# Optimization experiments

Measured on AMD Instinct MI355X. Metric: run time of the kernel, lower is better.

Reference implementation:

```python
import jax, jax.numpy as jnp
import numpy as np

B, A, RF, F = 4096, 128, 128, 128  # batch, max_atom, res_n_features, n_features


def setup_inputs() -> dict:
    key = jax.random.key(0)
    k1, k2, k3, k4 = jax.random.split(key, 4)
    node_features = jax.random.normal(k1, (B, A, F), dtype=jnp.float32)
    residual_features = jax.random.normal(k2, (B, A, RF), dtype=jnp.float32)
    # Glorot-style init for the residual transform weight
    scale = jnp.sqrt(6.0 / (RF + F)).astype(jnp.float32)
    w = jax.random.uniform(k3, (RF, F), dtype=jnp.float32, minval=-scale, maxval=scale)
    # mol_slice[g] = [n_atoms_g, n_features]; atom counts vary per graph (ragged)
    atoms = jax.random.randint(k4, (B,), 1, A + 1, dtype=jnp.int64)
    mol_slice = jnp.stack([atoms, jnp.full((B,), F, dtype=jnp.int64)], axis=1)
    return {"node_features": node_features, "residual_features": residual_features,
            "w": w, "mol_slice": mol_slice}


def reference(node_features, residual_features, w, mol_slice):
    # Original: per-graph slice to [M_g, F], x_res @ w + x, pad back to max_atom,
    # then relu. Equivalent masked batched form: rows >= M_g become zeros.
    M = mol_slice[:, 0]  # [B] atom counts
    row_mask = (jnp.arange(A)[None, :] < M[:, None])[:, :, None]  # [B, A, 1]
    y = jnp.einsum('bar,rf->baf', residual_features, w) + node_features  # [B, A, F]
    return jnp.where(row_mask, jax.nn.relu(y), jnp.zeros((), dtype=y.dtype))
```

## Files before the change

kernel.cpp:

```cpp
#include <hip/hip_runtime.h>


typedef __bf16 bf16x8 __attribute__((ext_vector_type(8)));
typedef float f32x4 __attribute__((ext_vector_type(4)));

static_assert(sizeof(bf16x8) == 16, "bf16x8 must be 16B");
static_assert(sizeof(f32x4) == 16, "f32x4 must be 16B");

__global__ __launch_bounds__(256) void wT_kernel(const float* __restrict__ w,
                                                 __bf16* __restrict__ wT) {
    int i = blockIdx.x * 256 + threadIdx.x;
    int f = i >> 7;
    int r = i & 127;
    wT[i] = (__bf16)w[r * 128 + f];
}

__global__ __launch_bounds__(256) void blockend_kernel(
    const float* __restrict__ node,
    const float* __restrict__ resid,
    const __bf16* __restrict__ wT,
    const int*   __restrict__ mol,
    float*       __restrict__ out)
{
    const int b    = blockIdx.x;
    const int t    = threadIdx.x;
    const int wave = t >> 6;
    const int lane = t & 63;
    const int quad = lane >> 4;
    const int m16  = lane & 15;

    const int M      = mol[2 * b];
    const int a_base = wave * 32;

    const size_t base = (size_t)b * (128 * 128);
    float* outW = out + base + (size_t)a_base * 128;

    if (M <= a_base) {
        f32x4 z = {0.f, 0.f, 0.f, 0.f};
        f32x4* p = (f32x4*)outW;
#pragma unroll
        for (int it = 0; it < 16; ++it)
            p[it * 64 + lane] = z;
        return;
    }

    const float* residW = resid + base + (size_t)a_base * 128;
    const float* nodeW  = node  + base + (size_t)a_base * 128;

    f32x4 acc[2][8];
#pragma unroll
    for (int nt = 0; nt < 2; ++nt)
#pragma unroll
        for (int ft = 0; ft < 8; ++ft)
            acc[nt][ft] = (f32x4){0.f, 0.f, 0.f, 0.f};

#pragma unroll
    for (int kk = 0; kk < 4; ++kk) {
        const int k0 = kk * 32 + quad * 8;

        bf16x8 rfrag[2];
#pragma unroll
        for (int nt = 0; nt < 2; ++nt) {
            const float* ap = residW + (nt * 16 + m16) * 128 + k0;
            f32x4 lo = *(const f32x4*)ap;
            f32x4 hi = *(const f32x4*)(ap + 4);
            bf16x8 v;
            v[0] = (__bf16)lo[0]; v[1] = (__bf16)lo[1];
            v[2] = (__bf16)lo[2]; v[3] = (__bf16)lo[3];
            v[4] = (__bf16)hi[0]; v[5] = (__bf16)hi[1];
            v[6] = (__bf16)hi[2]; v[7] = (__bf16)hi[3];
            rfrag[nt] = v;
        }

#pragma unroll
        for (int ft = 0; ft < 8; ++ft) {
            bf16x8 wfrag = *(const bf16x8*)(wT + (ft * 16 + m16) * 128 + k0);
#pragma unroll
            for (int nt = 0; nt < 2; ++nt)
                acc[nt][ft] = __builtin_amdgcn_mfma_f32_16x16x32_bf16(
                    wfrag, rfrag[nt], acc[nt][ft], 0, 0, 0);
        }
    }

#pragma unroll
    for (int nt = 0; nt < 2; ++nt) {
        const int a_local = nt * 16 + m16;
        const bool active = (a_base + a_local) < M;
#pragma unroll
        for (int ft = 0; ft < 8; ++ft) {
            const int off = a_local * 128 + ft * 16 + quad * 4;
            f32x4 v = {0.f, 0.f, 0.f, 0.f};
            if (active) {
                f32x4 nd = *(const f32x4*)(nodeW + off);
#pragma unroll
                for (int i = 0; i < 4; ++i) {
                    float x = acc[nt][ft][i] + nd[i];
                    v[i] = x > 0.f ? x : 0.f;
                }
            }
            *(f32x4*)(outW + off) = v;
        }
    }
}

extern "C" void kernel_launch(void* const* d_in, const int* in_sizes, int n_in,
                              void* d_out, int out_size, void* d_ws, size_t ws_size,
                              hipStream_t stream) {
    const float* node  = (const float*)d_in[0];
    const float* resid = (const float*)d_in[1];
    const float* w     = (const float*)d_in[2];
    const int*   mol   = (const int*)d_in[3];
    float*       out   = (float*)d_out;
    __bf16*      wT    = (__bf16*)d_ws;

    wT_kernel<<<64, 256, 0, stream>>>(w, wT);
    blockend_kernel<<<4096, 256, 0, stream>>>(node, resid, wT, mol, out);
}
```

Measured before the change: 575.1 us.

## Stage weights in LDS, process two graphs per block, skip masked row loads

```diff
diff --git a/kernel.cpp b/kernel.cpp
--- a/kernel.cpp
+++ b/kernel.cpp
@@ -7,6 +7,8 @@
 static_assert(sizeof(bf16x8) == 16, "bf16x8 must be 16B");
 static_assert(sizeof(f32x4) == 16, "f32x4 must be 16B");
 
+#define PB 2
+
 __global__ __launch_bounds__(256) void wT_kernel(const float* __restrict__ w,
                                                  __bf16* __restrict__ wT) {
     int i = blockIdx.x * 256 + threadIdx.x;
@@ -15,90 +17,113 @@
     wT[i] = (__bf16)w[r * 128 + f];
 }
 
-__global__ __launch_bounds__(256) void blockend_kernel(
+__global__ __launch_bounds__(256, 4) void blockend_kernel(
     const float* __restrict__ node,
     const float* __restrict__ resid,
-    const __bf16* __restrict__ wT,
+    const __bf16* __restrict__ wTg,
     const int*   __restrict__ mol,
     float*       __restrict__ out)
 {
-    const int b    = blockIdx.x;
+    __shared__ bf16x8 wlds[2048];
+
     const int t    = threadIdx.x;
     const int wave = t >> 6;
     const int lane = t & 63;
     const int quad = lane >> 4;
     const int m16  = lane & 15;
 
-    const int M      = mol[2 * b];
+#pragma unroll
+    for (int i = 0; i < 8; ++i) {
+        int c   = t + i * 256;
+        int f   = c >> 4;
+        int pos = c & 15;
+        bf16x8 v = *(const bf16x8*)(wTg + c * 8);
+        int s = (f >> 4) * 256 + (pos >> 2) * 64 + (pos & 3) * 16 + (f & 15);
+        wlds[s] = v;
+    }
+    __syncthreads();
+
     const int a_base = wave * 32;
 
-    const size_t base = (size_t)b * (128 * 128);
-    float* outW = out + base + (size_t)a_base * 128;
+    for (int mi = 0; mi < PB; ++mi) {
+        const int b = blockIdx.x * PB + mi;
+        const int M = mol[2 * b];
+        const size_t base = (size_t)b * (128 * 128);
+        float* outW = out + base + (size_t)a_base * 128;
 
-    if (M <= a_base) {
-        f32x4 z = {0.f, 0.f, 0.f, 0.f};
-        f32x4* p = (f32x4*)outW;
+        if (M <= a_base) {
+            f32x4 z = {0.f, 0.f, 0.f, 0.f};
+            f32x4* p = (f32x4*)outW;
 #pragma unroll
-        for (int it = 0; it < 16; ++it)
-            p[it * 64 + lane] = z;
-        return;
-    }
+            for (int it = 0; it < 16; ++it)
+                __builtin_nontemporal_store(z, p + it * 64 + lane);
+            continue;
+        }
 
-    const float* residW = resid + base + (size_t)a_base * 128;
-    const float* nodeW  = node  + base + (size_t)a_base * 128;
+        bf16x8 rfrag[2][4];
+#pragma unroll
+        for (int nt = 0; nt < 2; ++nt) {
+            const int row  = a_base + nt * 16 + m16;
+            const bool act = row < M;
+            const float* rp = resid + base + (size_t)row * 128 + quad * 8;
+#pragma unroll
+            for (int kk = 0; kk < 4; ++kk) {
+                f32x4 lo = {0.f, 0.f, 0.f, 0.f};
+                f32x4 hi = {0.f, 0.f, 0.f, 0.f};
+                if (act) {
+                    lo = *(const f32x4*)(rp + kk * 32);
+                    hi = *(const f32x4*)(rp + kk * 32 + 4);
+                }
+                bf16x8 v;
+                v[0] = (__bf16)lo[0]; v[1] = (__bf16)lo[1];
+                v[2] = (__bf16)lo[2]; v[3] = (__bf16)lo[3];
+                v[4] = (__bf16)hi[0]; v[5] = (__bf16)hi[1];
+                v[6] = (__bf16)hi[2]; v[7] = (__bf16)hi[3];
+                rfrag[nt][kk] = v;
+            }
+        }
 
-    f32x4 acc[2][8];
-#pragma unroll
-    for (int nt = 0; nt < 2; ++nt)
-#pragma unroll
-        for (int ft = 0; ft < 8; ++ft)
-            acc[nt][ft] = (f32x4){0.f, 0.f, 0.f, 0.f};
+        const float* nodeW = node + base + (size_t)a_base * 128;
 
 #pragma unroll
-    for (int kk = 0; kk < 4; ++kk) {
-        const int k0 = kk * 32 + quad * 8;
-
-        bf16x8 rfrag[2];
+        for (int h = 0; h < 2; ++h) {
+            f32x4 acc[2][4];
 #pragma unroll
-        for (int nt = 0; nt < 2; ++nt) {
-            const float* ap = residW + (nt * 16 + m16) * 128 + k0;
-            f32x4 lo = *(const f32x4*)ap;
-            f32x4 hi = *(const f32x4*)(ap + 4);
-            bf16x8 v;
-            v[0] = (__bf16)lo[0]; v[1] = (__bf16)lo[1];
-            v[2] = (__bf16)lo[2]; v[3] = (__bf16)lo[3];
-            v[4] = (__bf16)hi[0]; v[5] = (__bf16)hi[1];
-            v[6] = (__bf16)hi[2]; v[7] = (__bf16)hi[3];
-            rfrag[nt] = v;
-        }
+            for (int nt = 0; nt < 2; ++nt)
+#pragma unroll
+                for (int fl = 0; fl < 4; ++fl)
+                    acc[nt][fl] = (f32x4){0.f, 0.f, 0.f, 0.f};
 
 #pragma unroll
-        for (int ft = 0; ft < 8; ++ft) {
-            bf16x8 wfrag = *(const bf16x8*)(wT + (ft * 16 + m16) * 128 + k0);
+            for (int kk = 0; kk < 4; ++kk)
 #pragma unroll
-            for (int nt = 0; nt < 2; ++nt)
-                acc[nt][ft] = __builtin_amdgcn_mfma_f32_16x16x32_bf16(
-                    wfrag, rfrag[nt], acc[nt][ft], 0, 0, 0);
-        }
-    }
+                for (int fl = 0; fl < 4; ++fl) {
+                    bf16x8 wf = wlds[((h * 4 + fl) * 4 + kk) * 64 + lane];
+                    acc[0][fl] = __builtin_amdgcn_mfma_f32_16x16x32_bf16(
+                        wf, rfrag[0][kk], acc[0][fl], 0, 0, 0);
+                    acc[1][fl] = __builtin_amdgcn_mfma_f32_16x16x32_bf16(
+                        wf, rfrag[1][kk], acc[1][fl], 0, 0, 0);
+                }
 
 #pragma unroll
-    for (int nt = 0; nt < 2; ++nt) {
-        const int a_local = nt * 16 + m16;
-        const bool active = (a_base + a_local) < M;
+            for (int nt = 0; nt < 2; ++nt) {
+                const int a_local = nt * 16 + m16;
+                const bool active = (a_base + a_local) < M;
 #pragma unroll
-        for (int ft = 0; ft < 8; ++ft) {
-            const int off = a_local * 128 + ft * 16 + quad * 4;
-            f32x4 v = {0.f, 0.f, 0.f, 0.f};
-            if (active) {
-                f32x4 nd = *(const f32x4*)(nodeW + off);
+                for (int fl = 0; fl < 4; ++fl) {
+                    const int off = a_local * 128 + (h * 4 + fl) * 16 + quad * 4;
+                    f32x4 v = {0.f, 0.f, 0.f, 0.f};
+                    if (active) {
+                        f32x4 nd = *(const f32x4*)(nodeW + off);
 #pragma unroll
-                for (int i = 0; i < 4; ++i) {
-                    float x = acc[nt][ft][i] + nd[i];
-                    v[i] = x > 0.f ? x : 0.f;
+                        for (int i = 0; i < 4; ++i) {
+                            float x = acc[nt][fl][i] + nd[i];
+                            v[i] = x > 0.f ? x : 0.f;
+                        }
+                    }
+                    __builtin_nontemporal_store(v, (f32x4*)(outW + off));
                 }
             }
-            *(f32x4*)(outW + off) = v;
         }
     }
 }
@@ -114,5 +139,5 @@
     __bf16*      wT    = (__bf16*)d_ws;
 
     wT_kernel<<<64, 256, 0, stream>>>(w, wT);
-    blockend_kernel<<<4096, 256, 0, stream>>>(node, resid, wT, mol, out);
+    blockend_kernel<<<4096 / PB, 256, 0, stream>>>(node, resid, wT, mol, out);
 }
```

After: 589.0 us. 1.02x slower.
